# Kernel optimization log

Measured on AMD Instinct MI355X. Metric: run time of the kernel, lower is better.

Reference implementation:

```python
import jax, jax.numpy as jnp
import numpy as np

DIM = 768
NUM_HEADS = 12
KERNEL = 3
DILATIONS = (1, 2, 3)


def setup_inputs() -> dict:
    key = jax.random.key(0)
    k1, k2, k3, k4 = jax.random.split(key, 4)
    B, N, C = 4, 4096, DIM
    return {
        "x": jax.random.normal(k1, (B, N, C), jnp.float32),
        "w_qkv": jax.random.normal(k2, (3 * C, C), jnp.float32) * 0.02,
        "w_proj": jax.random.normal(k3, (C, C), jnp.float32) * 0.02,
        "b_proj": jax.random.normal(k4, (C,), jnp.float32) * 0.02,
    }


def _dilate_attention(q, k, v, dilation, head_dim, kernel):
    # q,k,v: [B, d, N] where d = C / num_dilation
    B, d, N = q.shape
    h = d // head_dim
    scale = head_dim ** -0.5
    qh = q.reshape(B, h, head_dim, N)
    kh = k.reshape(B, h, head_dim, N)
    vh = v.reshape(B, h, head_dim, N)
    pad = dilation * (kernel - 1) // 2

    def windows(t):
        # gather the `kernel` dilated neighbors along N with zero padding
        tp = jnp.pad(t, ((0, 0), (0, 0), (0, 0), (pad, pad)))
        return jnp.stack([tp[..., j * dilation: j * dilation + N] for j in range(kernel)], axis=3)  # [B,h,hd,kernel,N]

    k_win = windows(kh)
    v_win = windows(vh)
    scores = jnp.einsum('bhdn,bhdkn->bhnk', qh, k_win) * scale  # [B,h,N,kernel]
    # Torch nn.Unfold on the [B,d,N,1] 'image' yields kernel*kernel columns;
    # only the center width-column is real, the rest are zero padding -> score 0.
    kk = kernel * kernel
    center = (kernel - 1) // 2
    scores_full = jnp.zeros(scores.shape[:3] + (kk,), scores.dtype).at[..., center::kernel].set(scores)
    probs = jax.nn.softmax(scores_full, axis=-1)  # zero-key columns dilute the softmax, faithfully
    probs_real = probs[..., center::kernel]  # [B,h,N,kernel]; zero-key columns multiply zero values
    out = jnp.einsum('bhnk,bhdkn->bhnd', probs_real, v_win)  # [B,h,N,hd]
    return out.transpose(0, 2, 1, 3).reshape(B, N, d)


def reference(x, w_qkv, w_proj, b_proj):
    B, N, C = x.shape
    nd = len(DILATIONS)
    head_dim = C // NUM_HEADS
    # [B,N,3C] -> [B,N,3,nd,C/nd] -> [nd,3,B,C/nd,N]
    qkv = (x @ w_qkv.T).reshape(B, N, 3, nd, C // nd).transpose(3, 2, 0, 4, 1)
    outs = [_dilate_attention(qkv[i, 0], qkv[i, 1], qkv[i, 2], DILATIONS[i], head_dim, KERNEL)
            for i in range(nd)]
    xo = jnp.stack(outs, axis=2).reshape(B, N, C)  # [B,N,nd,d] -> [B,N,C]
    xo = xo @ w_proj.T + b_proj
    # matches torch return (x, x2=None, v, k, q); x2 omitted (is_decoder=False)
    return (xo, qkv[:, 2], qkv[:, 1], qkv[:, 0])
```

## Files before the change

kernel.cpp:

```cpp
#include <hip/hip_runtime.h>

typedef __attribute__((ext_vector_type(8))) short bf16x8;
typedef __attribute__((ext_vector_type(4))) float f32x4;

#define SZQKV 12582912

__device__ __forceinline__ unsigned short f2bf(float f) {
    unsigned int u = __float_as_uint(f);
    unsigned int r = (u + 0x7FFFu + ((u >> 16) & 1u)) >> 16;
    return (unsigned short)r;
}

#define GLDS16(g, l) __builtin_amdgcn_global_load_lds( \
    (const __attribute__((address_space(1))) unsigned int*)(g), \
    (__attribute__((address_space(3))) unsigned int*)(l), 16, 0, 0)

__global__ void cast_all(const float* __restrict__ x,
                         const float* __restrict__ wqkv,
                         const float* __restrict__ wproj,
                         unsigned short* __restrict__ dst) {
    const int T1 = 12582912;
    const int T2 = T1 + 1769472;
    const int T3 = T2 + 589824;
    int stride = gridDim.x * blockDim.x * 4;
    for (int base = (blockIdx.x * blockDim.x + threadIdx.x) * 4; base < T3; base += stride) {
        const float* src; int off;
        if (base < T1)      { src = x;     off = base; }
        else if (base < T2) { src = wqkv;  off = base - T1; }
        else                { src = wproj; off = base - T2; }
        float4 v = *(const float4*)(src + off);
        ushort4 o;
        o.x = f2bf(v.x); o.y = f2bf(v.y); o.z = f2bf(v.z); o.w = f2bf(v.w);
        *(ushort4*)(dst + base) = o;
    }
}

__global__ __launch_bounds__(256) void gemm_qkv(const unsigned short* __restrict__ A,
                                                const unsigned short* __restrict__ Bw,
                                                float* __restrict__ dout) {
    __shared__ unsigned short lA[128 * 32];
    __shared__ unsigned short lB[128 * 32];
    const int m0 = blockIdx.x * 128;
    const int n0 = blockIdx.y * 128;
    const int t = threadIdx.x;
    const int lane = t & 63;
    const int w = t >> 6;
    const int wm = w >> 1, wn = w & 1;
    f32x4 acc[4][4] = {};

    for (int k0 = 0; k0 < 768; k0 += 32) {
#pragma unroll
        for (int i = 0; i < 2; ++i) {
            int elt = (i * 256 + t) * 8;
            int row = elt >> 5;
            int kk  = elt & 31;
            GLDS16(A  + (size_t)(m0 + row) * 768 + k0 + kk, &lA[elt]);
            GLDS16(Bw + (size_t)(n0 + row) * 768 + k0 + kk, &lB[elt]);
        }
        __syncthreads();
        bf16x8 av[4], bv[4];
#pragma unroll
        for (int mi = 0; mi < 4; ++mi)
            av[mi] = *(const bf16x8*)&lA[(wm * 64 + mi * 16 + (lane & 15)) * 32 + (lane >> 4) * 8];
#pragma unroll
        for (int ni = 0; ni < 4; ++ni)
            bv[ni] = *(const bf16x8*)&lB[(wn * 64 + ni * 16 + (lane & 15)) * 32 + (lane >> 4) * 8];
#pragma unroll
        for (int mi = 0; mi < 4; ++mi)
#pragma unroll
            for (int ni = 0; ni < 4; ++ni)
                acc[mi][ni] = __builtin_amdgcn_mfma_f32_16x16x32_bf16(av[mi], bv[ni], acc[mi][ni], 0, 0, 0);
        __syncthreads();
    }

    const int crow = (lane >> 4) * 4;
    const int ccol = lane & 15;
    const int b = m0 >> 12;
    const int n_base = m0 & 4095;
#pragma unroll
    for (int mi = 0; mi < 4; ++mi) {
        int n = n_base + wm * 64 + mi * 16 + crow;
#pragma unroll
        for (int ni = 0; ni < 4; ++ni) {
            int o = n0 + wn * 64 + ni * 16 + ccol;
            int sel = o / 768;
            int rem = o - sel * 768;
            float* dst = dout + (size_t)(3 - sel) * SZQKV
                       + ((size_t)((rem >> 8) * 4 + b) * 256 + (rem & 255)) * 4096 + n;
            *(f32x4*)dst = acc[mi][ni];
        }
    }
}

__global__ __launch_bounds__(256) void attn_kernel(const float* __restrict__ qkv,
                                                   unsigned short* __restrict__ attnbf) {
    const int chunk = blockIdx.x;
    const int dil_i = blockIdx.y;
    const int b     = blockIdx.z;
    const int dil   = dil_i + 1;
    const int t  = threadIdx.x;
    const int h  = t >> 6;
    const int nl = t & 63;
    const int n  = chunk * 64 + nl;

    const size_t gb = (size_t)(dil_i * 4 + b) * 256 * 4096;
    const float* Q = qkv + (size_t)3 * SZQKV + gb;
    const float* K = qkv + (size_t)2 * SZQKV + gb;
    const float* V = qkv + (size_t)1 * SZQKV + gb;

    const int nm = n - dil, np = n + dil;
    const bool vm = (nm >= 0), vp = (np < 4096);
    const int nmc = vm ? nm : 0, npc = vp ? np : 4095;

    float s0 = 0.f, s1 = 0.f, s2 = 0.f;
    {
        const float* qrow = Q + (size_t)h * 64 * 4096;
        const float* krow = K + (size_t)h * 64 * 4096;
        for (int d = 0; d < 64; ++d) {
            float q = qrow[n];
            s0 += q * krow[nmc];
            s1 += q * krow[n];
            s2 += q * krow[npc];
            qrow += 4096; krow += 4096;
        }
    }
    s0 = vm ? s0 * 0.125f : 0.f;
    s1 *= 0.125f;
    s2 = vp ? s2 * 0.125f : 0.f;
    float mx = fmaxf(0.f, fmaxf(s0, fmaxf(s1, s2)));
    float e0 = __expf(s0 - mx), e1 = __expf(s1 - mx), e2 = __expf(s2 - mx);
    float den = e0 + e1 + e2 + 6.f * __expf(-mx);
    float inv = 1.f / den;
    float p0 = vm ? e0 * inv : 0.f;
    float p1 = e1 * inv;
    float p2 = vp ? e2 * inv : 0.f;

    __shared__ unsigned short lout[256][65];
    {
        const float* vrow = V + (size_t)h * 64 * 4096;
        for (int d = 0; d < 64; ++d) {
            float o = p0 * vrow[nmc] + p1 * vrow[n] + p2 * vrow[npc];
            lout[h * 64 + d][nl] = f2bf(o);
            vrow += 4096;
        }
    }
    __syncthreads();

#pragma unroll
    for (int i = 0; i < 8; ++i) {
        int linear = i * 256 + t;
        int nn   = linear >> 5;
        int cblk = linear & 31;
        union { unsigned short u[8]; f32x4 v; } tt;
#pragma unroll
        for (int j = 0; j < 8; ++j) tt.u[j] = lout[cblk * 8 + j][nn];
        unsigned short* dst = attnbf + (size_t)(b * 4096 + chunk * 64 + nn) * 768
                            + dil_i * 256 + cblk * 8;
        *(f32x4*)dst = tt.v;
    }
}

__global__ __launch_bounds__(256) void gemm_proj(const unsigned short* __restrict__ A,
                                                 const unsigned short* __restrict__ Bw,
                                                 const float* __restrict__ bias,
                                                 float* __restrict__ out) {
    __shared__ unsigned short lA[128 * 32];
    __shared__ unsigned short lB[128 * 32];
    const int m0 = blockIdx.x * 128;
    const int n0 = blockIdx.y * 128;
    const int t = threadIdx.x;
    const int lane = t & 63;
    const int w = t >> 6;
    const int wm = w >> 1, wn = w & 1;
    f32x4 acc[4][4] = {};

    for (int k0 = 0; k0 < 768; k0 += 32) {
#pragma unroll
        for (int i = 0; i < 2; ++i) {
            int elt = (i * 256 + t) * 8;
            int row = elt >> 5;
            int kk  = elt & 31;
            GLDS16(A  + (size_t)(m0 + row) * 768 + k0 + kk, &lA[elt]);
            GLDS16(Bw + (size_t)(n0 + row) * 768 + k0 + kk, &lB[elt]);
        }
        __syncthreads();
        bf16x8 av[4], bv[4];
#pragma unroll
        for (int mi = 0; mi < 4; ++mi)
            av[mi] = *(const bf16x8*)&lA[(wm * 64 + mi * 16 + (lane & 15)) * 32 + (lane >> 4) * 8];
#pragma unroll
        for (int ni = 0; ni < 4; ++ni)
            bv[ni] = *(const bf16x8*)&lB[(wn * 64 + ni * 16 + (lane & 15)) * 32 + (lane >> 4) * 8];
#pragma unroll
        for (int mi = 0; mi < 4; ++mi)
#pragma unroll
            for (int ni = 0; ni < 4; ++ni)
                acc[mi][ni] = __builtin_amdgcn_mfma_f32_16x16x32_bf16(av[mi], bv[ni], acc[mi][ni], 0, 0, 0);
        __syncthreads();
    }

    const int crow = (lane >> 4) * 4;
    const int ccol = lane & 15;
#pragma unroll
    for (int mi = 0; mi < 4; ++mi) {
        int m = m0 + wm * 64 + mi * 16 + crow;
#pragma unroll
        for (int ni = 0; ni < 4; ++ni) {
            int o = n0 + wn * 64 + ni * 16 + ccol;
            float bb = bias[o];
#pragma unroll
            for (int r = 0; r < 4; ++r)
                out[(size_t)(m + r) * 768 + o] = acc[mi][ni][r] + bb;
        }
    }
}

extern "C" void kernel_launch(void* const* d_in, const int* in_sizes, int n_in,
                              void* d_out, int out_size, void* d_ws, size_t ws_size,
                              hipStream_t stream) {
    const float* x     = (const float*)d_in[0];
    const float* wqkv  = (const float*)d_in[1];
    const float* wproj = (const float*)d_in[2];
    const float* bproj = (const float*)d_in[3];
    float* out = (float*)d_out;

    unsigned short* xbf     = (unsigned short*)d_ws;
    unsigned short* wqkvbf  = xbf + 12582912;
    unsigned short* wprojbf = wqkvbf + 1769472;
    unsigned short* attnbf  = wprojbf + 589824;

    cast_all<<<2048, 256, 0, stream>>>(x, wqkv, wproj, xbf);

    dim3 g1(128, 18);
    gemm_qkv<<<g1, 256, 0, stream>>>(xbf, wqkvbf, out);

    attn_kernel<<<dim3(64, 3, 4), 256, 0, stream>>>(out, attnbf);

    dim3 g2(128, 6);
    gemm_proj<<<g2, 256, 0, stream>>>(attnbf, wprojbf, bproj, out);
}
```

Baseline: 192.0 us.

## Merge GEMMs into a triple-buffered, swizzled 256x128 tile kernel with XCD remap

Both GEMMs now run through one templated kernel that uses 512-thread blocks on 256x128 tiles with a BK of 32. Global-to-LDS loads are triple-buffered with explicit vmcnt waits, so the next K-tiles load while the current one feeds the MFMAs. The LDS rows are XOR-swizzled to cut bank conflicts, and block IDs are remapped across the 8 XCDs for cache locality. The aim is to hide memory latency and remove one of the two barriers' stalls, at the cost of more LDS per block and hand-managed waitcnt correctness.

```diff
diff --git a/kernel.cpp b/kernel.cpp
--- a/kernel.cpp
+++ b/kernel.cpp
@@ -35,59 +35,123 @@
     }
 }
 
-__global__ __launch_bounds__(256) void gemm_qkv(const unsigned short* __restrict__ A,
-                                                const unsigned short* __restrict__ Bw,
-                                                float* __restrict__ dout) {
-    __shared__ unsigned short lA[128 * 32];
-    __shared__ unsigned short lB[128 * 32];
-    const int m0 = blockIdx.x * 128;
-    const int n0 = blockIdx.y * 128;
+template <int MODE>
+__global__ __launch_bounds__(512, 2) void gemm_big(const unsigned short* __restrict__ A,
+                                                   const unsigned short* __restrict__ Bw,
+                                                   const float* __restrict__ bias,
+                                                   float* __restrict__ dout,
+                                                   int nby) {
+    __shared__ unsigned char lds8[73728];
     const int t = threadIdx.x;
     const int lane = t & 63;
     const int w = t >> 6;
     const int wm = w >> 1, wn = w & 1;
+
+    const int cpx = gridDim.x >> 3;
+    const int orig = blockIdx.x;
+    const int wgid = (orig & 7) * cpx + (orig >> 3);
+    const int bx = wgid / nby, by = wgid - bx * nby;
+    const int m0 = bx * 256;
+    const int n0 = by * 128;
+
+    const unsigned char* Ab = (const unsigned char*)A;
+    const unsigned char* Bb = (const unsigned char*)Bw;
+
+    size_t aSrc0, aSrc1, bSrc;
+    {
+        int c0 = t, c1 = 512 + t;
+        int r0 = c0 >> 2, p0 = (c0 & 3) << 4;
+        int r1 = c1 >> 2, p1 = (c1 & 3) << 4;
+        aSrc0 = (size_t)(m0 + r0) * 1536 + (p0 ^ ((r0 & 3) << 4));
+        aSrc1 = (size_t)(m0 + r1) * 1536 + (p1 ^ ((r1 & 3) << 4));
+        int rb = t >> 2, pb = (t & 3) << 4;
+        bSrc  = (size_t)(n0 + rb) * 1536 + (pb ^ ((rb & 3) << 4));
+    }
+
+    int aOff[4], bOff[4];
+#pragma unroll
+    for (int mi = 0; mi < 4; ++mi) {
+        int row = wm * 64 + mi * 16 + (lane & 15);
+        aOff[mi] = row * 64 + ((((lane >> 4) << 4)) ^ ((row & 3) << 4));
+    }
+#pragma unroll
+    for (int ni = 0; ni < 4; ++ni) {
+        int row = wn * 64 + ni * 16 + (lane & 15);
+        bOff[ni] = 16384 + row * 64 + ((((lane >> 4) << 4)) ^ ((row & 3) << 4));
+    }
+
     f32x4 acc[4][4] = {};
 
-    for (int k0 = 0; k0 < 768; k0 += 32) {
-#pragma unroll
-        for (int i = 0; i < 2; ++i) {
-            int elt = (i * 256 + t) * 8;
-            int row = elt >> 5;
-            int kk  = elt & 31;
-            GLDS16(A  + (size_t)(m0 + row) * 768 + k0 + kk, &lA[elt]);
-            GLDS16(Bw + (size_t)(n0 + row) * 768 + k0 + kk, &lB[elt]);
-        }
-        __syncthreads();
+#define STAGE(bi, kt) do { \
+    unsigned char* dst_ = lds8 + (bi) * 24576; \
+    GLDS16(Ab + aSrc0 + (size_t)(kt) * 64, dst_ + t * 16); \
+    GLDS16(Ab + aSrc1 + (size_t)(kt) * 64, dst_ + 8192 + t * 16); \
+    GLDS16(Bb + bSrc  + (size_t)(kt) * 64, dst_ + 16384 + t * 16); \
+} while (0)
+
+    STAGE(0, 0);
+    STAGE(1, 1);
+    int bi = 0;
+    for (int kt = 0; kt < 24; ++kt) {
+        if (kt < 22) {
+            int si = bi + 2; if (si >= 3) si -= 3;
+            STAGE(si, kt + 2);
+            asm volatile("s_waitcnt vmcnt(6)" ::: "memory");
+        } else if (kt == 22) {
+            asm volatile("s_waitcnt vmcnt(3)" ::: "memory");
+        } else {
+            asm volatile("s_waitcnt vmcnt(0)" ::: "memory");
+        }
+        __builtin_amdgcn_s_barrier();
+        asm volatile("" ::: "memory");
+        const unsigned char* base = lds8 + bi * 24576;
         bf16x8 av[4], bv[4];
 #pragma unroll
-        for (int mi = 0; mi < 4; ++mi)
-            av[mi] = *(const bf16x8*)&lA[(wm * 64 + mi * 16 + (lane & 15)) * 32 + (lane >> 4) * 8];
-#pragma unroll
-        for (int ni = 0; ni < 4; ++ni)
-            bv[ni] = *(const bf16x8*)&lB[(wn * 64 + ni * 16 + (lane & 15)) * 32 + (lane >> 4) * 8];
+        for (int mi = 0; mi < 4; ++mi) av[mi] = *(const bf16x8*)(base + aOff[mi]);
+#pragma unroll
+        for (int ni = 0; ni < 4; ++ni) bv[ni] = *(const bf16x8*)(base + bOff[ni]);
 #pragma unroll
         for (int mi = 0; mi < 4; ++mi)
 #pragma unroll
             for (int ni = 0; ni < 4; ++ni)
                 acc[mi][ni] = __builtin_amdgcn_mfma_f32_16x16x32_bf16(av[mi], bv[ni], acc[mi][ni], 0, 0, 0);
-        __syncthreads();
-    }
+        asm volatile("s_waitcnt lgkmcnt(0)" ::: "memory");
+        __builtin_amdgcn_s_barrier();
+        asm volatile("" ::: "memory");
+        ++bi; if (bi == 3) bi = 0;
+    }
+#undef STAGE
 
     const int crow = (lane >> 4) * 4;
     const int ccol = lane & 15;
-    const int b = m0 >> 12;
-    const int n_base = m0 & 4095;
-#pragma unroll
-    for (int mi = 0; mi < 4; ++mi) {
-        int n = n_base + wm * 64 + mi * 16 + crow;
-#pragma unroll
-        for (int ni = 0; ni < 4; ++ni) {
-            int o = n0 + wn * 64 + ni * 16 + ccol;
-            int sel = o / 768;
-            int rem = o - sel * 768;
-            float* dst = dout + (size_t)(3 - sel) * SZQKV
-                       + ((size_t)((rem >> 8) * 4 + b) * 256 + (rem & 255)) * 4096 + n;
-            *(f32x4*)dst = acc[mi][ni];
+    if (MODE == 0) {
+        const int b = m0 >> 12;
+        const int n_base = m0 & 4095;
+#pragma unroll
+        for (int mi = 0; mi < 4; ++mi) {
+            int n = n_base + wm * 64 + mi * 16 + crow;
+#pragma unroll
+            for (int ni = 0; ni < 4; ++ni) {
+                int o = n0 + wn * 64 + ni * 16 + ccol;
+                int sel = o / 768;
+                int rem = o - sel * 768;
+                float* dst = dout + (size_t)(3 - sel) * SZQKV
+                           + ((size_t)((rem >> 8) * 4 + b) * 256 + (rem & 255)) * 4096 + n;
+                *(f32x4*)dst = acc[mi][ni];
+            }
+        }
+    } else {
+#pragma unroll
+        for (int mi = 0; mi < 4; ++mi) {
+            int m = m0 + wm * 64 + mi * 16 + crow;
+#pragma unroll
+            for (int ni = 0; ni < 4; ++ni) {
+                int o = n0 + wn * 64 + ni * 16 + ccol;
+                float bb = bias[o];
+#pragma unroll
+                for (int r = 0; r < 4; ++r)
+                    dout[(size_t)(m + r) * 768 + o] = acc[mi][ni][r] + bb;
+            }
         }
     }
 }
@@ -160,61 +224,6 @@
     }
 }
 
-__global__ __launch_bounds__(256) void gemm_proj(const unsigned short* __restrict__ A,
-                                                 const unsigned short* __restrict__ Bw,
-                                                 const float* __restrict__ bias,
-                                                 float* __restrict__ out) {
-    __shared__ unsigned short lA[128 * 32];
-    __shared__ unsigned short lB[128 * 32];
-    const int m0 = blockIdx.x * 128;
-    const int n0 = blockIdx.y * 128;
-    const int t = threadIdx.x;
-    const int lane = t & 63;
-    const int w = t >> 6;
-    const int wm = w >> 1, wn = w & 1;
-    f32x4 acc[4][4] = {};
-
-    for (int k0 = 0; k0 < 768; k0 += 32) {
-#pragma unroll
-        for (int i = 0; i < 2; ++i) {
-            int elt = (i * 256 + t) * 8;
-            int row = elt >> 5;
-            int kk  = elt & 31;
-            GLDS16(A  + (size_t)(m0 + row) * 768 + k0 + kk, &lA[elt]);
-            GLDS16(Bw + (size_t)(n0 + row) * 768 + k0 + kk, &lB[elt]);
-        }
-        __syncthreads();
-        bf16x8 av[4], bv[4];
-#pragma unroll
-        for (int mi = 0; mi < 4; ++mi)
-            av[mi] = *(const bf16x8*)&lA[(wm * 64 + mi * 16 + (lane & 15)) * 32 + (lane >> 4) * 8];
-#pragma unroll
-        for (int ni = 0; ni < 4; ++ni)
-            bv[ni] = *(const bf16x8*)&lB[(wn * 64 + ni * 16 + (lane & 15)) * 32 + (lane >> 4) * 8];
-#pragma unroll
-        for (int mi = 0; mi < 4; ++mi)
-#pragma unroll
-            for (int ni = 0; ni < 4; ++ni)
-                acc[mi][ni] = __builtin_amdgcn_mfma_f32_16x16x32_bf16(av[mi], bv[ni], acc[mi][ni], 0, 0, 0);
-        __syncthreads();
-    }
-
-    const int crow = (lane >> 4) * 4;
-    const int ccol = lane & 15;
-#pragma unroll
-    for (int mi = 0; mi < 4; ++mi) {
-        int m = m0 + wm * 64 + mi * 16 + crow;
-#pragma unroll
-        for (int ni = 0; ni < 4; ++ni) {
-            int o = n0 + wn * 64 + ni * 16 + ccol;
-            float bb = bias[o];
-#pragma unroll
-            for (int r = 0; r < 4; ++r)
-                out[(size_t)(m + r) * 768 + o] = acc[mi][ni][r] + bb;
-        }
-    }
-}
-
 extern "C" void kernel_launch(void* const* d_in, const int* in_sizes, int n_in,
                               void* d_out, int out_size, void* d_ws, size_t ws_size,
                               hipStream_t stream) {
@@ -231,11 +240,9 @@
 
     cast_all<<<2048, 256, 0, stream>>>(x, wqkv, wproj, xbf);
 
-    dim3 g1(128, 18);
-    gemm_qkv<<<g1, 256, 0, stream>>>(xbf, wqkvbf, out);
+    gemm_big<0><<<dim3(64 * 18), 512, 0, stream>>>(xbf, wqkvbf, nullptr, out, 18);
 
     attn_kernel<<<dim3(64, 3, 4), 256, 0, stream>>>(out, attnbf);
 
-    dim3 g2(128, 6);
-    gemm_proj<<<g2, 256, 0, stream>>>(attnbf, wprojbf, bproj, out);
-}
+    gemm_big<1><<<dim3(64 * 6), 512, 0, stream>>>(attnbf, wprojbf, bproj, out, 6);
+}
```

Measured after the change: 173.0 us. 1.11x faster.
